# Kernel optimization log

Measured on AMD Instinct MI355X. Metric: run time of the kernel, lower is better.

Reference implementation:

```python
import jax, jax.numpy as jnp
import numpy as np

B, T, L, H, NH, F, V, K = 8, 128, 12, 768, 12, 3072, 30522, 5
DH = H // NH
START, STOP = 3, 4  # tag_to_idx['<START>'], tag_to_idx['<STOP>']


def _ln(x, s, b):
    m = jnp.mean(x, -1, keepdims=True)
    v = jnp.var(x, -1, keepdims=True)
    return (x - m) * jax.lax.rsqrt(v + 1e-12) * s + b


def setup_inputs() -> dict:
    key = jax.random.key(0)
    ks = jax.random.split(key, 16)
    sc = 0.02
    rn = lambda k, shp: jax.random.normal(k, shp, jnp.float32) * sc
    inp = {
        'sentence': jax.random.randint(ks[0], (B, T), 0, V),
        'sentence_mask': jnp.ones((B, T), jnp.int32),
        'word_emb': rn(ks[1], (V, H)),
        'pos_emb': rn(ks[2], (T, H)),
        'type_emb': rn(ks[3], (2, H)),
        'emb_ln_s': jnp.ones((H,), jnp.float32),
        'emb_ln_b': jnp.zeros((H,), jnp.float32),
        'Wqkv': rn(ks[4], (L, H, 3 * H)), 'bqkv': jnp.zeros((L, 3 * H), jnp.float32),
        'Wo': rn(ks[5], (L, H, H)), 'bo': jnp.zeros((L, H), jnp.float32),
        'ln1_s': jnp.ones((L, H), jnp.float32), 'ln1_b': jnp.zeros((L, H), jnp.float32),
        'W1': rn(ks[6], (L, H, F)), 'b1': jnp.zeros((L, F), jnp.float32),
        'W2': rn(ks[7], (L, F, H)), 'b2': jnp.zeros((L, H), jnp.float32),
        'ln2_s': jnp.ones((L, H), jnp.float32), 'ln2_b': jnp.zeros((L, H), jnp.float32),
        'Wt': rn(ks[8], (H, K)), 'bt': jnp.zeros((K,), jnp.float32),
    }
    trans = jax.random.normal(ks[9], (K, K), jnp.float32)
    # transitions[START, :] = -10000 ; transitions[:, STOP] = -10000
    trans = trans.at[START, :].set(-10000.0).at[:, STOP].set(-10000.0)
    inp['transitions'] = trans
    return inp


def _bert_feats(sentence, sentence_mask, word_emb, pos_emb, type_emb,
                emb_ln_s, emb_ln_b, Wqkv, bqkv, Wo, bo, ln1_s, ln1_b,
                W1, b1, W2, b2, ln2_s, ln2_b, Wt, bt):
    # embeddings (token_type_ids=None -> all zeros)
    x = word_emb[sentence] + pos_emb[None, :, :] + type_emb[0][None, None, :]
    x = _ln(x, emb_ln_s, emb_ln_b)
    # additive attention bias from padding mask
    bias = (1.0 - sentence_mask.astype(jnp.float32))[:, None, None, :] * -10000.0
    inv_sqrt_dh = 1.0 / np.sqrt(DH)

    def layer(h, p):
        wqkv, bqk, wo, bo_, s1, sb1, w1, wb1, w2, wb2, s2, sb2 = p
        qkv = h @ wqkv + bqk
        q, k, v = jnp.split(qkv, 3, axis=-1)
        q = q.reshape(B, T, NH, DH)
        k = k.reshape(B, T, NH, DH)
        v = v.reshape(B, T, NH, DH)
        att = jnp.einsum('bqhd,bkhd->bhqk', q, k) * inv_sqrt_dh + bias
        att = jax.nn.softmax(att, axis=-1)
        ctx = jnp.einsum('bhqk,bkhd->bqhd', att, v).reshape(B, T, H)
        h = _ln(h + ctx @ wo + bo_, s1, sb1)
        ff = jax.nn.gelu(h @ w1 + wb1) @ w2 + wb2
        h = _ln(h + ff, s2, sb2)
        return h, None

    x, _ = jax.lax.scan(layer, x, (Wqkv, bqkv, Wo, bo, ln1_s, ln1_b,
                                   W1, b1, W2, b2, ln2_s, ln2_b))
    # dropout(p=0.2) is identity at inference
    return x @ Wt + bt  # [B, T, K]


def _viterbi(feats, transitions):
    # feats: [B, T, K]; transitions[to, from]
    init = jnp.full((B, K), -10000.0, feats.dtype).at[:, START].set(0.0)

    def fwd_step(ld, feat_t):
        m = transitions[None, :, :] + ld[:, None, :]  # [B, K(to), K(from)]
        best = jnp.max(m, axis=-1)
        psi_t = jnp.argmax(m, axis=-1)
        return best + feat_t, psi_t

    feats_t = jnp.swapaxes(feats, 0, 1)  # [T, B, K]
    ld, psis = jax.lax.scan(fwd_step, init, feats_t[1:])  # psis: [T-1, B, K]
    score = jnp.max(ld, axis=-1)          # [B]
    last = jnp.argmax(ld, axis=-1)        # [B]

    def bwd_step(p, psi_t):
        prev = jnp.take_along_axis(psi_t, p[:, None], axis=-1)[:, 0]
        return prev, prev

    _, rest = jax.lax.scan(bwd_step, last, psis, reverse=True)  # [T-1, B]
    path = jnp.concatenate([rest, last[None, :]], axis=0).T     # [B, T]
    return score, path


def reference(sentence, sentence_mask, word_emb, pos_emb, type_emb,
              emb_ln_s, emb_ln_b, Wqkv, bqkv, Wo, bo, ln1_s, ln1_b,
              W1, b1, W2, b2, ln2_s, ln2_b, Wt, bt, transitions):
    feats = _bert_feats(sentence, sentence_mask, word_emb, pos_emb, type_emb,
                        emb_ln_s, emb_ln_b, Wqkv, bqkv, Wo, bo, ln1_s, ln1_b,
                        W1, b1, W2, b2, ln2_s, ln2_b, Wt, bt)
    score, path = _viterbi(feats, transitions)
    return score, path
```

## Files before the change

### kernel.cpp

```cpp
#include <hip/hip_runtime.h>
#include <cstdint>
#include <cstddef>

#define BB 8
#define TT 128
#define LL 12
#define HH 768
#define NHH 12
#define DHH 64
#define FFI 3072
#define KT 5
#define START_TAG 3
#define MTOK (BB*TT)

#define LQS 1769472u
#define LOS 589824u
#define L1S 2359296u
#define L2S 2359296u

typedef _Float16 f16x8 __attribute__((ext_vector_type(8)));
typedef _Float16 f16x4 __attribute__((ext_vector_type(4)));
typedef float f32x4 __attribute__((ext_vector_type(4)));

__device__ __forceinline__ void gl_lds16(const _Float16* g, _Float16* l) {
    __builtin_amdgcn_global_load_lds(
        (const __attribute__((address_space(1))) unsigned int*)g,
        (__attribute__((address_space(3))) unsigned int*)l, 16, 0, 0);
}

__device__ __forceinline__ float gelu_f(float x) {
    float c = 0.7978845608028654f * (x + 0.044715f * x * x * x);
    return 0.5f * x * (1.f + tanhf(c));
}

__device__ __forceinline__ void write_h_planes(const float* rowbuf, int tok,
                                               _Float16* dh, _Float16* dl, int c) {
    int kb = c >> 2;
    int rowm = tok & 127, mb = tok >> 7;
    int koct = c & 3;
    int p = rowm * 4 + (koct ^ (rowm & 3));
    size_t tb = ((size_t)(mb * 24 + kb)) * 4096;
    f16x8 vh, vl;
#pragma unroll
    for (int j = 0; j < 8; ++j) {
        float x = rowbuf[c * 8 + j];
        _Float16 hi = (_Float16)x;
        vh[j] = hi;
        vl[j] = (_Float16)((x - (float)hi) * 4096.f);
    }
    *(f16x8*)(dh + tb + (size_t)p * 8) = vh;
    *(f16x8*)(dl + tb + (size_t)p * 8) = vl;
}

__global__ __launch_bounds__(256) void embed_ln_kernel(
    const int* __restrict__ sentence,
    const float* __restrict__ word_emb,
    const float* __restrict__ pos_emb,
    const float* __restrict__ type_emb,
    const float* __restrict__ ln_s,
    const float* __restrict__ ln_b,
    float* __restrict__ h,
    _Float16* __restrict__ dh, _Float16* __restrict__ dl)
{
    int tok = blockIdx.x;
    int t = tok % TT;
    int id = sentence[tok];
    const float* we = word_emb + (size_t)id * HH;
    const float* pe = pos_emb + (size_t)t * HH;

    __shared__ float rowbuf[HH];
    __shared__ float rs_[4], rss_[4];
    float x[3];
    float s = 0.f, ss = 0.f;
#pragma unroll
    for (int i = 0; i < 3; ++i) {
        int d = threadIdx.x + i * 256;
        float v = we[d] + pe[d] + type_emb[d];
        x[i] = v; s += v; ss += v * v;
    }
    for (int o = 32; o; o >>= 1) { s += __shfl_down(s, o); ss += __shfl_down(ss, o); }
    int wid = threadIdx.x >> 6;
    if ((threadIdx.x & 63) == 0) { rs_[wid] = s; rss_[wid] = ss; }
    __syncthreads();
    s = rs_[0] + rs_[1] + rs_[2] + rs_[3];
    ss = rss_[0] + rss_[1] + rss_[2] + rss_[3];
    float mean = s * (1.f / HH);
    float var = ss * (1.f / HH) - mean * mean;
    float rstd = rsqrtf(var + 1e-12f);
#pragma unroll
    for (int i = 0; i < 3; ++i) {
        int d = threadIdx.x + i * 256;
        float y = (x[i] - mean) * rstd * ln_s[d] + ln_b[d];
        h[(size_t)tok * HH + d] = y;
        rowbuf[d] = y;
    }
    __syncthreads();
    if (threadIdx.x < 96) write_h_planes(rowbuf, tok, dh, dl, threadIdx.x);
}

template<int FEATS>
__global__ __launch_bounds__(256) void add_ln_red_kernel(
    float* __restrict__ h, const float* __restrict__ parts,
    const float* __restrict__ bias,
    const float* __restrict__ ln_s, const float* __restrict__ ln_b,
    _Float16* __restrict__ dh, _Float16* __restrict__ dl,
    const float* __restrict__ Wt, const float* __restrict__ bt,
    float* __restrict__ feats)
{
    int tok = blockIdx.x;
    __shared__ float rowbuf[HH];
    __shared__ float rs_[4], rss_[4];
    float x[3];
    float s = 0.f, ss = 0.f;
#pragma unroll
    for (int i = 0; i < 3; ++i) {
        int d = threadIdx.x + i * 256;
        size_t idx = (size_t)tok * HH + d;
        float delta = parts[idx] + parts[idx + (size_t)MTOK * HH]
                    + parts[idx + 2 * (size_t)MTOK * HH] + parts[idx + 3 * (size_t)MTOK * HH]
                    + bias[d];
        float v = h[idx] + delta;
        x[i] = v; s += v; ss += v * v;
    }
    for (int o = 32; o; o >>= 1) { s += __shfl_down(s, o); ss += __shfl_down(ss, o); }
    int wid = threadIdx.x >> 6;
    if ((threadIdx.x & 63) == 0) { rs_[wid] = s; rss_[wid] = ss; }
    __syncthreads();
    s = rs_[0] + rs_[1] + rs_[2] + rs_[3];
    ss = rss_[0] + rss_[1] + rss_[2] + rss_[3];
    float mean = s * (1.f / HH);
    float var = ss * (1.f / HH) - mean * mean;
    float rstd = rsqrtf(var + 1e-12f);
    float yv[3];
#pragma unroll
    for (int i = 0; i < 3; ++i) {
        int d = threadIdx.x + i * 256;
        float y = (x[i] - mean) * rstd * ln_s[d] + ln_b[d];
        yv[i] = y;
        if constexpr (!FEATS) {
            h[(size_t)tok * HH + d] = y;
            rowbuf[d] = y;
        }
    }
    if constexpr (!FEATS) {
        __syncthreads();
        if (threadIdx.x < 96) write_h_planes(rowbuf, tok, dh, dl, threadIdx.x);
    } else {
        float pt[5] = {0.f, 0.f, 0.f, 0.f, 0.f};
#pragma unroll
        for (int i = 0; i < 3; ++i) {
            int d = threadIdx.x + i * 256;
#pragma unroll
            for (int t = 0; t < 5; ++t) pt[t] += yv[i] * Wt[d * 5 + t];
        }
#pragma unroll
        for (int t = 0; t < 5; ++t)
            for (int o = 32; o; o >>= 1) pt[t] += __shfl_down(pt[t], o);
        __shared__ float fred[4][5];
        if ((threadIdx.x & 63) == 0)
#pragma unroll
            for (int t = 0; t < 5; ++t) fred[wid][t] = pt[t];
        __syncthreads();
        if (threadIdx.x < 5) {
            float fs = fred[0][threadIdx.x] + fred[1][threadIdx.x]
                     + fred[2][threadIdx.x] + fred[3][threadIdx.x] + bt[threadIdx.x];
            feats[tok * 5 + threadIdx.x] = fs;
        }
    }
}

template<int ALL>
__global__ __launch_bounds__(256) void wconv_kernel(
    const float* __restrict__ Wqkv, const float* __restrict__ Wo,
    const float* __restrict__ W1, const float* __restrict__ W2,
    _Float16* __restrict__ qh, _Float16* __restrict__ ql,
    _Float16* __restrict__ oh, _Float16* __restrict__ ol,
    _Float16* __restrict__ f1h, _Float16* __restrict__ f1l,
    _Float16* __restrict__ f2h, _Float16* __restrict__ f2l)
{
    int bb = blockIdx.x;
    int l = ALL ? bb / 3456 : 0;
    int b = ALL ? bb % 3456 : bb;
    const float* src; _Float16 *dh, *dl; int N, kTi, idx;
    if (b < 864)       { idx = b;        src = Wqkv + (size_t)l * 768 * 2304; dh = qh  + (size_t)l * LQS; dl = ql  + (size_t)l * LQS; N = 2304; kTi = 24; }
    else if (b < 1152) { idx = b - 864;  src = Wo   + (size_t)l * 768 * 768;  dh = oh  + (size_t)l * LOS; dl = ol  + (size_t)l * LOS; N = 768;  kTi = 24; }
    else if (b < 2304) { idx = b - 1152; src = W1   + (size_t)l * 768 * 3072; dh = f1h + (size_t)l * L1S; dl = f1l + (size_t)l * L1S; N = 3072; kTi = 24; }
    else               { idx = b - 2304; src = W2   + (size_t)l * 3072 * 768; dh = f2h + (size_t)l * L2S; dl = f2l + (size_t)l * L2S; N = 768;  kTi = 96; }
    int nb = idx / kTi, kb = idx % kTi;

    __shared__ float tile[32][65];
    const float* s0 = src + (size_t)(kb * 32) * N + nb * 64;
#pragma unroll
    for (int i = 0; i < 8; ++i) {
        int q = threadIdx.x + i * 256;
        int kk = q >> 6, n = q & 63;
        tile[kk][n] = s0[(size_t)kk * N + n];
    }
    __syncthreads();
    int p = threadIdx.x;
    int n = p >> 2, koct = (p & 3) ^ (n & 3);
    f16x8 vh, vl;
#pragma unroll
    for (int j = 0; j < 8; ++j) {
        float x = tile[koct * 8 + j][n];
        _Float16 hi = (_Float16)x;
        vh[j] = hi;
        vl[j] = (_Float16)((x - (float)hi) * 4096.f);
    }
    size_t tb = (size_t)idx * 2048;
    *(f16x8*)(dh + tb + (size_t)p * 8) = vh;
    *(f16x8*)(dl + tb + (size_t)p * 8) = vl;
}

template<int MODE>
__global__ __launch_bounds__(256) void mfma_gemm(
    const _Float16* __restrict__ Ah, const _Float16* __restrict__ Al,
    const _Float16* __restrict__ Bh, const _Float16* __restrict__ Bl,
    const float* __restrict__ bias, float* __restrict__ outF,
    _Float16* __restrict__ o1h, _Float16* __restrict__ o1l,
    _Float16* __restrict__ o2h, _Float16* __restrict__ o2l,
    int N, int kTi, int kpz)
{
    constexpr bool TRANS = (MODE >= 2);
    __shared__ _Float16 lds[2][12288];
    int tid = threadIdx.x, lane = tid & 63, w = tid >> 6;
    int wm = w >> 1, wn = w & 1;
    int mb = blockIdx.y, nb = blockIdx.x;
    int ktBeg = TRANS ? 0 : blockIdx.z * kpz;
    int ktEnd = TRANS ? kTi : ktBeg + kpz;

    const _Float16 *aTh, *aTl, *bTh, *bTl;
    if constexpr (!TRANS) {
        aTh = Ah + (size_t)mb * kTi * 4096;
        aTl = Al + (size_t)mb * kTi * 4096;
        bTh = Bh + (size_t)nb * kTi * 2048;
        bTl = Bl + (size_t)nb * kTi * 2048;
    } else {
        aTh = Ah + (size_t)(2 * mb) * kTi * 2048;
        aTl = Al + (size_t)(2 * mb) * kTi * 2048;
        bTh = Bh + (size_t)(nb >> 1) * kTi * 4096 + (nb & 1) * 2048;
        bTl = Bl + (size_t)(nb >> 1) * kTi * 4096 + (nb & 1) * 2048;
    }

    f32x4 acch[4][2], accc[4][2];
#pragma unroll
    for (int i = 0; i < 4; ++i)
#pragma unroll
        for (int j = 0; j < 2; ++j) { acch[i][j] = (f32x4)0.f; accc[i][j] = (f32x4)0.f; }

    auto stage = [&](int buf, int kt) {
#pragma unroll
        for (int j = 0; j < 6; ++j) {
            int i = w * 6 + j;
            const _Float16* src;
            if constexpr (!TRANS) {
                if (i < 8)       src = aTh + (size_t)kt * 4096 + i * 512;
                else if (i < 16) src = aTl + (size_t)kt * 4096 + (i - 8) * 512;
                else if (i < 20) src = bTh + (size_t)kt * 2048 + (i - 16) * 512;
                else             src = bTl + (size_t)kt * 2048 + (i - 20) * 512;
            } else {
                if (i < 8)       src = aTh + (size_t)(i >> 2) * kTi * 2048 + (size_t)kt * 2048 + (i & 3) * 512;
                else if (i < 16) src = aTl + (size_t)((i - 8) >> 2) * kTi * 2048 + (size_t)kt * 2048 + ((i - 8) & 3) * 512;
                else if (i < 20) src = bTh + (size_t)kt * 4096 + (i - 16) * 512;
                else             src = bTl + (size_t)kt * 4096 + (i - 20) * 512;
            }
            gl_lds16(src + lane * 8, &lds[buf][i * 512]);
        }
    };

    stage(0, ktBeg);
    stage(1, ktBeg + 1);
    int lm = lane & 15, lk = lane >> 4;
    for (int kt = ktBeg; kt < ktEnd; ++kt) {
        int cur = (kt - ktBeg) & 1;
        if (kt + 1 < ktEnd) { asm volatile("s_waitcnt vmcnt(6)" ::: "memory"); }
        else                { asm volatile("s_waitcnt vmcnt(0)" ::: "memory"); }
        __builtin_amdgcn_s_barrier();
        __builtin_amdgcn_sched_barrier(0);
        const char* lb = (const char*)&lds[cur][0];
        f16x8 ahf[4], alf[4], bhf[2], blf[2];
#pragma unroll
        for (int mi = 0; mi < 4; ++mi) {
            int row = wm * 64 + mi * 16 + lm;
            int off = (row * 64 + lk * 16) ^ ((row & 3) << 4);
            ahf[mi] = *(const f16x8*)(lb + off);
            alf[mi] = *(const f16x8*)(lb + 8192 + off);
        }
#pragma unroll
        for (int ni = 0; ni < 2; ++ni) {
            int nr = wn * 32 + ni * 16 + lm;
            int off = (nr * 64 + lk * 16) ^ ((nr & 3) << 4);
            bhf[ni] = *(const f16x8*)(lb + 16384 + off);
            blf[ni] = *(const f16x8*)(lb + 20480 + off);
        }
#pragma unroll
        for (int mi = 0; mi < 4; ++mi)
#pragma unroll
            for (int ni = 0; ni < 2; ++ni) {
                acch[mi][ni] = __builtin_amdgcn_mfma_f32_16x16x32_f16(ahf[mi], bhf[ni], acch[mi][ni], 0, 0, 0);
                accc[mi][ni] = __builtin_amdgcn_mfma_f32_16x16x32_f16(ahf[mi], blf[ni], accc[mi][ni], 0, 0, 0);
                accc[mi][ni] = __builtin_amdgcn_mfma_f32_16x16x32_f16(alf[mi], bhf[ni], accc[mi][ni], 0, 0, 0);
            }
        __builtin_amdgcn_sched_barrier(0);
        __builtin_amdgcn_s_barrier();
        if (kt + 2 < ktEnd) stage(cur, kt + 2);
    }

    const float inv = 1.0f / 4096.0f;
    if constexpr (MODE == 0) {
        float* Cz = outF + (size_t)blockIdx.z * 1024 * N;
#pragma unroll
        for (int mi = 0; mi < 4; ++mi)
#pragma unroll
            for (int ni = 0; ni < 2; ++ni) {
                int col = nb * 64 + wn * 32 + ni * 16 + lm;
                int r0 = mb * 128 + wm * 64 + mi * 16 + lk * 4;
#pragma unroll
                for (int j = 0; j < 4; ++j)
                    Cz[(size_t)(r0 + j) * N + col] = acch[mi][ni][j] + accc[mi][ni][j] * inv;
            }
    } else if constexpr (MODE == 2) {
        int region = mb / 6;
#pragma unroll
        for (int mi = 0; mi < 4; ++mi)
#pragma unroll
            for (int ni = 0; ni < 2; ++ni) {
                int n = mb * 128 + wm * 64 + mi * 16 + lk * 4;
                int tok = nb * 64 + wn * 32 + ni * 16 + lm;
                float4 bv = *(const float4*)(bias + n);
                float v[4];
#pragma unroll
                for (int j = 0; j < 4; ++j)
                    v[j] = acch[mi][ni][j] + accc[mi][ni][j] * inv + (&bv.x)[j];
                int b = tok >> 7, q = tok & 127;
                if (region < 2) {
                    int hh2 = (n >> 6) % 12, d = n & 63;
                    size_t img = (size_t)(b * 12 + hh2);
                    _Float16* dsth = (region == 0) ? o1h : o2h;
                    _Float16* dstl = (region == 0) ? o1l : o2l;
                    int byteo = q * 128 + ((d * 2) ^ ((q & 7) << 4));
                    f16x4 hi, lo;
#pragma unroll
                    for (int j = 0; j < 4; ++j) {
                        _Float16 hv = (_Float16)v[j];
                        hi[j] = hv; lo[j] = (_Float16)((v[j] - (float)hv) * 4096.f);
                    }
                    *(f16x4*)((char*)dsth + img * 16384 + byteo) = hi;
                    *(f16x4*)((char*)dstl + img * 16384 + byteo) = lo;
                } else {
                    int hh2 = (n - 1536) >> 6, d = n & 63;
                    float* vdst = outF + (size_t)(b * 12 + hh2) * 8192;
#pragma unroll
                    for (int j = 0; j < 4; ++j)
                        vdst[(size_t)(d + j) * 128 + q] = v[j];
                }
            }
    } else {
#pragma unroll
        for (int mi = 0; mi < 4; ++mi)
#pragma unroll
            for (int ni = 0; ni < 2; ++ni) {
                int n = mb * 128 + wm * 64 + mi * 16 + lk * 4;
                int tok = nb * 64 + wn * 32 + ni * 16 + lm;
                float4 bv = *(const float4*)(bias + n);
                int mbt = tok >> 7, rowm = tok & 127;
                int kb = n >> 5, koct = (n >> 3) & 3, half = (n >> 2) & 1;
                size_t eo = ((size_t)(mbt * 96 + kb)) * 4096
                          + (size_t)(rowm * 4 + (koct ^ (rowm & 3))) * 8 + half * 4;
                f16x4 hi, lo;
#pragma unroll
                for (int j = 0; j < 4; ++j) {
                    float x = gelu_f(acch[mi][ni][j] + accc[mi][ni][j] * inv + (&bv.x)[j]);
                    _Float16 hv = (_Float16)x;
                    hi[j] = hv; lo[j] = (_Float16)((x - (float)hv) * 4096.f);
                }
                *(f16x4*)(o1h + eo) = hi;
                *(f16x4*)(o1l + eo) = lo;
            }
    }
}

__global__ __launch_bounds__(256, 1) void attn_mfma(
    const _Float16* __restrict__ Qp_h, const _Float16* __restrict__ Qp_l,
    const _Float16* __restrict__ Kp_h, const _Float16* __restrict__ Kp_l,
    const float* __restrict__ vT, const int* __restrict__ mask,
    _Float16* __restrict__ cA_h, _Float16* __restrict__ cA_l)
{
    __shared__ __align__(16) char sm[82432];
    char* Kh  = sm;             char* Klo = sm + 16384;
    char* Qh  = sm + 32768;     char* Qlo = sm + 40960;
    char* Ph  = sm;             char* Plo = sm + 16384;
    char* Vth = sm + 49152;     char* Vtl = sm + 65536;
    float* biasf = (float*)(sm + 81920);

    int bx = blockIdx.x;
    int bh = bx >> 1, qh2 = bx & 1;
    int b = bh / 12, h = bh % 12;
    int q0 = qh2 * 64;
    int tid = threadIdx.x, lane = tid & 63, wv = tid >> 6;
    int lm = lane & 15, g = lane >> 4;
    int qr = wv * 16 + lm;
    const float inv = 1.0f / 4096.0f;

    {
        const _Float16* Ksh = Kp_h + (size_t)bh * 8192;
        const _Float16* Ksl = Kp_l + (size_t)bh * 8192;
        const _Float16* Qsh = Qp_h + (size_t)bh * 8192 + (size_t)q0 * 64;
        const _Float16* Qsl = Qp_l + (size_t)bh * 8192 + (size_t)q0 * 64;
#pragma unroll
        for (int i = 0; i < 4; ++i) {
            gl_lds16(Ksh + (size_t)(i * 256 + tid) * 8, (_Float16*)(Kh  + (i * 256 + tid) * 16));
            gl_lds16(Ksl + (size_t)(i * 256 + tid) * 8, (_Float16*)(Klo + (i * 256 + tid) * 16));
        }
#pragma unroll
        for (int i = 0; i < 2; ++i) {
            gl_lds16(Qsh + (size_t)(i * 256 + tid) * 8, (_Float16*)(Qh  + (i * 256 + tid) * 16));
            gl_lds16(Qsl + (size_t)(i * 256 + tid) * 8, (_Float16*)(Qlo + (i * 256 + tid) * 16));
        }
    }
    if (tid < 128) biasf[tid] = (1.f - (float)mask[b * 128 + tid]) * -10000.f;
    __syncthreads();

    f32x4 ah[8], ac[8];
#pragma unroll
    for (int i = 0; i < 8; ++i) { ah[i] = (f32x4)0.f; ac[i] = (f32x4)0.f; }
    __builtin_amdgcn_s_setprio(1);
#pragma unroll
    for (int ks = 0; ks < 2; ++ks) {
        int qoff = qr * 128 + ((ks * 64 + g * 16) ^ ((qr & 7) << 4));
        f16x8 q_h = *(const f16x8*)(Qh + qoff);
        f16x8 q_l = *(const f16x8*)(Qlo + qoff);
#pragma unroll
        for (int mf = 0; mf < 8; ++mf) {
            int kt = mf * 16 + lm;
            int koff = kt * 128 + ((ks * 64 + g * 16) ^ ((kt & 7) << 4));
            f16x8 k_h = *(const f16x8*)(Kh + koff);
            f16x8 k_l = *(const f16x8*)(Klo + koff);
            ah[mf] = __builtin_amdgcn_mfma_f32_16x16x32_f16(k_h, q_h, ah[mf], 0, 0, 0);
            ac[mf] = __builtin_amdgcn_mfma_f32_16x16x32_f16(k_h, q_l, ac[mf], 0, 0, 0);
            ac[mf] = __builtin_amdgcn_mfma_f32_16x16x32_f16(k_l, q_h, ac[mf], 0, 0, 0);
        }
    }
    __builtin_amdgcn_s_setprio(0);

    float kb_[8][4];
#pragma unroll
    for (int mf = 0; mf < 8; ++mf)
#pragma unroll
        for (int jj = 0; jj < 4; ++jj) kb_[mf][jj] = biasf[mf * 16 + g * 4 + jj];

    float pv_[8][4];
    float mx = -1e30f;
#pragma unroll
    for (int mf = 0; mf < 8; ++mf)
#pragma unroll
        for (int jj = 0; jj < 4; ++jj) {
            float s = (ah[mf][jj] + ac[mf][jj] * inv) * 0.125f + kb_[mf][jj];
            pv_[mf][jj] = s;
            mx = fmaxf(mx, s);
        }
    mx = fmaxf(mx, __shfl_xor(mx, 16));
    mx = fmaxf(mx, __shfl_xor(mx, 32));
    float sum = 0.f;
#pragma unroll
    for (int mf = 0; mf < 8; ++mf)
#pragma unroll
        for (int jj = 0; jj < 4; ++jj) {
            float e = expf(pv_[mf][jj] - mx);
            pv_[mf][jj] = e;
            sum += e;
        }
    sum += __shfl_xor(sum, 16);
    sum += __shfl_xor(sum, 32);
    float rs = 1.f / sum;
    __syncthreads();

#pragma unroll
    for (int mf = 0; mf < 8; ++mf) {
        f16x4 hi, lo;
#pragma unroll
        for (int jj = 0; jj < 4; ++jj) {
            float p = pv_[mf][jj] * rs;
            _Float16 hv = (_Float16)p;
            hi[jj] = hv; lo[jj] = (_Float16)((p - (float)hv) * 4096.f);
        }
        int byteo = qr * 256 + ((mf * 32 + g * 8) ^ ((qr & 7) << 4));
        *(f16x4*)(Ph + byteo) = hi;
        *(f16x4*)(Plo + byteo) = lo;
    }
    {
        int d = tid >> 2, tb = (tid & 3) * 32;
        const float* vsrc = vT + (size_t)bh * 8192 + (size_t)d * 128 + tb;
#pragma unroll
        for (int i = 0; i < 8; ++i) {
            float4 v = *(const float4*)(vsrc + i * 4);
            f16x4 hi, lo;
#pragma unroll
            for (int jj = 0; jj < 4; ++jj) {
                float x = (&v.x)[jj];
                _Float16 hv = (_Float16)x;
                hi[jj] = hv; lo[jj] = (_Float16)((x - (float)hv) * 4096.f);
            }
            int byteo = d * 256 + (((tb + i * 4) * 2) ^ ((d & 7) << 4));
            *(f16x4*)(Vth + byteo) = hi;
            *(f16x4*)(Vtl + byteo) = lo;
        }
    }
    __syncthreads();

    f32x4 ch[4], cc[4];
#pragma unroll
    for (int i = 0; i < 4; ++i) { ch[i] = (f32x4)0.f; cc[i] = (f32x4)0.f; }
    __builtin_amdgcn_s_setprio(1);
#pragma unroll
    for (int ks = 0; ks < 4; ++ks) {
        int poff = qr * 256 + ((ks * 64 + g * 16) ^ ((qr & 7) << 4));
        f16x8 p_h = *(const f16x8*)(Ph + poff);
        f16x8 p_l = *(const f16x8*)(Plo + poff);
#pragma unroll
        for (int mf = 0; mf < 4; ++mf) {
            int d = mf * 16 + lm;
            int voff = d * 256 + ((ks * 64 + g * 16) ^ ((d & 7) << 4));
            f16x8 vh = *(const f16x8*)(Vth + voff);
            f16x8 vl = *(const f16x8*)(Vtl + voff);
            ch[mf] = __builtin_amdgcn_mfma_f32_16x16x32_f16(vh, p_h, ch[mf], 0, 0, 0);
            cc[mf] = __builtin_amdgcn_mfma_f32_16x16x32_f16(vh, p_l, cc[mf], 0, 0, 0);
            cc[mf] = __builtin_amdgcn_mfma_f32_16x16x32_f16(vl, p_h, cc[mf], 0, 0, 0);
        }
    }
    __builtin_amdgcn_s_setprio(0);

    int q = q0 + qr;
#pragma unroll
    for (int mf = 0; mf < 4; ++mf) {
        int d0 = mf * 16 + g * 4;
        f16x4 hi, lo;
#pragma unroll
        for (int jj = 0; jj < 4; ++jj) {
            float x = ch[mf][jj] + cc[mf][jj] * inv;
            _Float16 hv = (_Float16)x;
            hi[jj] = hv; lo[jj] = (_Float16)((x - (float)hv) * 4096.f);
        }
        int kb = h * 2 + (d0 >> 5), koct = (d0 >> 3) & 3, half = (d0 >> 2) & 1;
        size_t eo = ((size_t)(b * 24 + kb)) * 4096
                  + (size_t)(q * 4 + (koct ^ (q & 3))) * 8 + half * 4;
        *(f16x4*)(cA_h + eo) = hi;
        *(f16x4*)(cA_l + eo) = lo;
    }
}

__global__ __launch_bounds__(64) void viterbi_kernel(
    const float* __restrict__ feats, const float* __restrict__ trans,
    float* __restrict__ out)
{
    __shared__ float tr[KT][KT];
    __shared__ unsigned char psi[TT - 1][BB][KT];
    int tid = threadIdx.x;
    if (tid < KT * KT) tr[tid / KT][tid % KT] = trans[tid];
    __syncthreads();
    if (tid < BB) {
        int b = tid;
        float ld[KT];
#pragma unroll
        for (int k = 0; k < KT; ++k) ld[k] = (k == START_TAG) ? 0.f : -10000.f;
        for (int t = 1; t < TT; ++t) {
            float nld[KT];
#pragma unroll
            for (int to = 0; to < KT; ++to) {
                float best = tr[to][0] + ld[0];
                int arg = 0;
#pragma unroll
                for (int fr = 1; fr < KT; ++fr) {
                    float v = tr[to][fr] + ld[fr];
                    if (v > best) { best = v; arg = fr; }
                }
                psi[t - 1][b][to] = (unsigned char)arg;
                nld[to] = best + feats[(size_t)(b * TT + t) * KT + to];
            }
#pragma unroll
            for (int k = 0; k < KT; ++k) ld[k] = nld[k];
        }
        float sc = ld[0]; int last = 0;
#pragma unroll
        for (int k = 1; k < KT; ++k) if (ld[k] > sc) { sc = ld[k]; last = k; }
        out[b] = sc;
        int p = last;
        out[BB + b * TT + (TT - 1)] = (float)last;
        for (int t = TT - 2; t >= 0; --t) {
            p = psi[t][b][p];
            out[BB + b * TT + t] = (float)p;
        }
    }
}

extern "C" void kernel_launch(void* const* d_in, const int* in_sizes, int n_in,
                              void* d_out, int out_size, void* d_ws, size_t ws_size,
                              hipStream_t stream) {
    const int*   sentence = (const int*)d_in[0];
    const int*   mask     = (const int*)d_in[1];
    const float* word_emb = (const float*)d_in[2];
    const float* pos_emb  = (const float*)d_in[3];
    const float* type_emb = (const float*)d_in[4];
    const float* emb_ln_s = (const float*)d_in[5];
    const float* emb_ln_b = (const float*)d_in[6];
    const float* Wqkv     = (const float*)d_in[7];
    const float* bqkv     = (const float*)d_in[8];
    const float* Wo       = (const float*)d_in[9];
    const float* bo       = (const float*)d_in[10];
    const float* ln1_s    = (const float*)d_in[11];
    const float* ln1_b    = (const float*)d_in[12];
    const float* W1       = (const float*)d_in[13];
    const float* b1       = (const float*)d_in[14];
    const float* W2       = (const float*)d_in[15];
    const float* b2       = (const float*)d_in[16];
    const float* ln2_s    = (const float*)d_in[17];
    const float* ln2_b    = (const float*)d_in[18];
    const float* Wt       = (const float*)d_in[19];
    const float* bt       = (const float*)d_in[20];
    const float* trans    = (const float*)d_in[21];

    char* base = (char*)d_ws;
    size_t off = 0;
    auto alloc = [&](size_t bytes) { void* p = base + off; off += (bytes + 255) & ~(size_t)255; return p; };

    const size_t planeElems = (size_t)(LQS + LOS + L1S + L2S);
    bool allL = ws_size >= (planeElems * 12 * 2 * 2 + (size_t)120 * 1024 * 1024);
    int NLL = allL ? 12 : 1;

    _Float16* wq_h = (_Float16*)alloc((size_t)LQS * NLL * 2);
    _Float16* wq_l = (_Float16*)alloc((size_t)LQS * NLL * 2);
    _Float16* wo_h = (_Float16*)alloc((size_t)LOS * NLL * 2);
    _Float16* wo_l = (_Float16*)alloc((size_t)LOS * NLL * 2);
    _Float16* w1_h = (_Float16*)alloc((size_t)L1S * NLL * 2);
    _Float16* w1_l = (_Float16*)alloc((size_t)L1S * NLL * 2);
    _Float16* w2_h = (_Float16*)alloc((size_t)L2S * NLL * 2);
    _Float16* w2_l = (_Float16*)alloc((size_t)L2S * NLL * 2);
    float* h       = (float*)alloc((size_t)MTOK * HH * 4);
    _Float16* hA_h = (_Float16*)alloc((size_t)MTOK * HH * 2);
    _Float16* hA_l = (_Float16*)alloc((size_t)MTOK * HH * 2);
    _Float16* Qp_h = (_Float16*)alloc((size_t)96 * 8192 * 2);
    _Float16* Qp_l = (_Float16*)alloc((size_t)96 * 8192 * 2);
    _Float16* Kp_h = (_Float16*)alloc((size_t)96 * 8192 * 2);
    _Float16* Kp_l = (_Float16*)alloc((size_t)96 * 8192 * 2);
    float* vT      = (float*)alloc((size_t)96 * 8192 * 4);
    _Float16* cA_h = (_Float16*)alloc((size_t)MTOK * HH * 2);
    _Float16* cA_l = (_Float16*)alloc((size_t)MTOK * HH * 2);
    _Float16* gA_h = (_Float16*)alloc((size_t)MTOK * FFI * 2);
    _Float16* gA_l = (_Float16*)alloc((size_t)MTOK * FFI * 2);
    float* parts   = (float*)alloc((size_t)4 * MTOK * HH * 4);
    float* featsb  = (float*)alloc((size_t)MTOK * KT * 4);

    embed_ln_kernel<<<MTOK, 256, 0, stream>>>(sentence, word_emb, pos_emb, type_emb,
                                              emb_ln_s, emb_ln_b, h, hA_h, hA_l);
    if (allL) {
        wconv_kernel<1><<<41472, 256, 0, stream>>>(
            Wqkv, Wo, W1, W2,
            wq_h, wq_l, wo_h, wo_l, w1_h, w1_l, w2_h, w2_l);
    }
    for (int l = 0; l < LL; ++l) {
        size_t qO = allL ? (size_t)l * LQS : 0;
        size_t oO = allL ? (size_t)l * LOS : 0;
        size_t f1O = allL ? (size_t)l * L1S : 0;
        size_t f2O = allL ? (size_t)l * L2S : 0;
        if (!allL) {
            wconv_kernel<0><<<3456, 256, 0, stream>>>(
                Wqkv + (size_t)l * 768 * 2304, Wo + (size_t)l * 768 * 768,
                W1 + (size_t)l * 768 * 3072, W2 + (size_t)l * 3072 * 768,
                wq_h, wq_l, wo_h, wo_l, w1_h, w1_l, w2_h, w2_l);
        }
        mfma_gemm<2><<<dim3(16, 18), 256, 0, stream>>>(
            wq_h + qO, wq_l + qO, hA_h, hA_l, bqkv + (size_t)l * 2304, vT,
            Qp_h, Qp_l, Kp_h, Kp_l, 0, 24, 24);
        attn_mfma<<<192, 256, 0, stream>>>(Qp_h, Qp_l, Kp_h, Kp_l, vT, mask, cA_h, cA_l);
        mfma_gemm<0><<<dim3(12, 8, 4), 256, 0, stream>>>(
            cA_h, cA_l, wo_h + oO, wo_l + oO, nullptr, parts,
            nullptr, nullptr, nullptr, nullptr, 768, 24, 6);
        add_ln_red_kernel<0><<<MTOK, 256, 0, stream>>>(
            h, parts, bo + (size_t)l * HH, ln1_s + (size_t)l * HH, ln1_b + (size_t)l * HH,
            hA_h, hA_l, nullptr, nullptr, nullptr);
        mfma_gemm<3><<<dim3(16, 24), 256, 0, stream>>>(
            w1_h + f1O, w1_l + f1O, hA_h, hA_l, b1 + (size_t)l * FFI, nullptr,
            gA_h, gA_l, nullptr, nullptr, 0, 24, 24);
        mfma_gemm<0><<<dim3(12, 8, 4), 256, 0, stream>>>(
            gA_h, gA_l, w2_h + f2O, w2_l + f2O, nullptr, parts,
            nullptr, nullptr, nullptr, nullptr, 768, 96, 24);
        if (l < LL - 1) {
            add_ln_red_kernel<0><<<MTOK, 256, 0, stream>>>(
                h, parts, b2 + (size_t)l * HH, ln2_s + (size_t)l * HH, ln2_b + (size_t)l * HH,
                hA_h, hA_l, nullptr, nullptr, nullptr);
        } else {
            add_ln_red_kernel<1><<<MTOK, 256, 0, stream>>>(
                h, parts, b2 + (size_t)l * HH, ln2_s + (size_t)l * HH, ln2_b + (size_t)l * HH,
                hA_h, hA_l, Wt, bt, featsb);
        }
    }
    viterbi_kernel<<<1, 64, 0, stream>>>(featsb, trans, (float*)d_out);
}
```

Measured before the change: 1.543 ms.

## Fuse all encoder layers into one persistent cooperative kernel with grid syncs

```diff
diff --git a/kernel.cpp b/kernel.cpp
--- a/kernel.cpp
+++ b/kernel.cpp
@@ -1,6 +1,9 @@
 #include <hip/hip_runtime.h>
+#include <hip/hip_cooperative_groups.h>
 #include <cstdint>
 #include <cstddef>
+
+namespace cg = cooperative_groups;
 
 #define BB 8
 #define TT 128
@@ -99,17 +102,18 @@
 }
 
 template<int FEATS>
-__global__ __launch_bounds__(256) void add_ln_red_kernel(
-    float* __restrict__ h, const float* __restrict__ parts,
-    const float* __restrict__ bias,
-    const float* __restrict__ ln_s, const float* __restrict__ ln_b,
-    _Float16* __restrict__ dh, _Float16* __restrict__ dl,
-    const float* __restrict__ Wt, const float* __restrict__ bt,
-    float* __restrict__ feats)
-{
-    int tok = blockIdx.x;
-    __shared__ float rowbuf[HH];
-    __shared__ float rs_[4], rss_[4];
+__device__ __forceinline__ void ln_body(
+    char* smemc, float* h, const float* parts, const float* bias,
+    const float* ln_s, const float* ln_b,
+    _Float16* dh, _Float16* dl,
+    const float* Wt, const float* bt, float* feats, int tok)
+{
+    float* rowbuf = (float*)smemc;
+    float* rs_ = (float*)(smemc + 3072);
+    float* rss_ = (float*)(smemc + 3088);
+    float (*fred)[5] = (float (*)[5])(smemc + 3104);
+    __syncthreads();
+
     float x[3];
     float s = 0.f, ss = 0.f;
 #pragma unroll
@@ -156,7 +160,6 @@
 #pragma unroll
         for (int t = 0; t < 5; ++t)
             for (int o = 32; o; o >>= 1) pt[t] += __shfl_down(pt[t], o);
-        __shared__ float fred[4][5];
         if ((threadIdx.x & 63) == 0)
 #pragma unroll
             for (int t = 0; t < 5; ++t) fred[wid][t] = pt[t];
@@ -167,6 +170,17 @@
             feats[tok * 5 + threadIdx.x] = fs;
         }
     }
+}
+
+template<int FEATS>
+__global__ __launch_bounds__(256) void add_ln_red_kernel(
+    float* h, const float* parts, const float* bias,
+    const float* ln_s, const float* ln_b,
+    _Float16* dh, _Float16* dl,
+    const float* Wt, const float* bt, float* feats)
+{
+    __shared__ __align__(16) char smem[3200];
+    ln_body<FEATS>(smem, h, parts, bias, ln_s, ln_b, dh, dl, Wt, bt, feats, blockIdx.x);
 }
 
 template<int ALL>
@@ -213,20 +227,20 @@
 }
 
 template<int MODE>
-__global__ __launch_bounds__(256) void mfma_gemm(
+__device__ __forceinline__ void gemm_tile(
+    char* smemc,
     const _Float16* __restrict__ Ah, const _Float16* __restrict__ Al,
     const _Float16* __restrict__ Bh, const _Float16* __restrict__ Bl,
     const float* __restrict__ bias, float* __restrict__ outF,
     _Float16* __restrict__ o1h, _Float16* __restrict__ o1l,
     _Float16* __restrict__ o2h, _Float16* __restrict__ o2l,
-    int N, int kTi, int kpz)
+    int N, int kTi, int kpz, int mb, int nb, int zz)
 {
     constexpr bool TRANS = (MODE >= 2);
-    __shared__ _Float16 lds[2][12288];
+    _Float16* lds = (_Float16*)smemc;
     int tid = threadIdx.x, lane = tid & 63, w = tid >> 6;
     int wm = w >> 1, wn = w & 1;
-    int mb = blockIdx.y, nb = blockIdx.x;
-    int ktBeg = TRANS ? 0 : blockIdx.z * kpz;
+    int ktBeg = TRANS ? 0 : zz * kpz;
     int ktEnd = TRANS ? kTi : ktBeg + kpz;
 
     const _Float16 *aTh, *aTl, *bTh, *bTl;
@@ -264,7 +278,7 @@
                 else if (i < 20) src = bTh + (size_t)kt * 4096 + (i - 16) * 512;
                 else             src = bTl + (size_t)kt * 4096 + (i - 20) * 512;
             }
-            gl_lds16(src + lane * 8, &lds[buf][i * 512]);
+            gl_lds16(src + lane * 8, &lds[buf * 12288 + i * 512]);
         }
     };
 
@@ -277,7 +291,7 @@
         else                { asm volatile("s_waitcnt vmcnt(0)" ::: "memory"); }
         __builtin_amdgcn_s_barrier();
         __builtin_amdgcn_sched_barrier(0);
-        const char* lb = (const char*)&lds[cur][0];
+        const char* lb = (const char*)&lds[cur * 12288];
         f16x8 ahf[4], alf[4], bhf[2], blf[2];
 #pragma unroll
         for (int mi = 0; mi < 4; ++mi) {
@@ -308,7 +322,7 @@
 
     const float inv = 1.0f / 4096.0f;
     if constexpr (MODE == 0) {
-        float* Cz = outF + (size_t)blockIdx.z * 1024 * N;
+        float* Cz = outF + (size_t)zz * 1024 * N;
 #pragma unroll
         for (int mi = 0; mi < 4; ++mi)
 #pragma unroll
@@ -380,20 +394,32 @@
     }
 }
 
-__global__ __launch_bounds__(256, 1) void attn_mfma(
+template<int MODE>
+__global__ __launch_bounds__(256) void mfma_gemm(
+    const _Float16* Ah, const _Float16* Al,
+    const _Float16* Bh, const _Float16* Bl,
+    const float* bias, float* outF,
+    _Float16* o1h, _Float16* o1l, _Float16* o2h, _Float16* o2l,
+    int N, int kTi, int kpz)
+{
+    __shared__ __align__(16) char smem[49152];
+    gemm_tile<MODE>(smem, Ah, Al, Bh, Bl, bias, outF, o1h, o1l, o2h, o2l,
+                    N, kTi, kpz, blockIdx.y, blockIdx.x, blockIdx.z);
+}
+
+__device__ __forceinline__ void attn_body(
+    char* sm,
     const _Float16* __restrict__ Qp_h, const _Float16* __restrict__ Qp_l,
     const _Float16* __restrict__ Kp_h, const _Float16* __restrict__ Kp_l,
     const float* __restrict__ vT, const int* __restrict__ mask,
-    _Float16* __restrict__ cA_h, _Float16* __restrict__ cA_l)
-{
-    __shared__ __align__(16) char sm[82432];
+    _Float16* __restrict__ cA_h, _Float16* __restrict__ cA_l, int bx)
+{
     char* Kh  = sm;             char* Klo = sm + 16384;
     char* Qh  = sm + 32768;     char* Qlo = sm + 40960;
     char* Ph  = sm;             char* Plo = sm + 16384;
     char* Vth = sm + 49152;     char* Vtl = sm + 65536;
     float* biasf = (float*)(sm + 81920);
 
-    int bx = blockIdx.x;
     int bh = bx >> 1, qh2 = bx & 1;
     int b = bh / 12, h = bh % 12;
     int q0 = qh2 * 64;
@@ -402,6 +428,7 @@
     int qr = wv * 16 + lm;
     const float inv = 1.0f / 4096.0f;
 
+    __syncthreads();
     {
         const _Float16* Ksh = Kp_h + (size_t)bh * 8192;
         const _Float16* Ksl = Kp_l + (size_t)bh * 8192;
@@ -546,6 +573,93 @@
                   + (size_t)(q * 4 + (koct ^ (q & 3))) * 8 + half * 4;
         *(f16x4*)(cA_h + eo) = hi;
         *(f16x4*)(cA_l + eo) = lo;
+    }
+}
+
+__global__ __launch_bounds__(256, 1) void attn_mfma(
+    const _Float16* Qp_h, const _Float16* Qp_l,
+    const _Float16* Kp_h, const _Float16* Kp_l,
+    const float* vT, const int* mask,
+    _Float16* cA_h, _Float16* cA_l)
+{
+    __shared__ __align__(16) char sm[82432];
+    attn_body(sm, Qp_h, Qp_l, Kp_h, Kp_l, vT, mask, cA_h, cA_l, blockIdx.x);
+}
+
+struct MegaArgs {
+    const int* mask;
+    const float *bqkv, *bo, *b1, *b2, *ln1_s, *ln1_b, *ln2_s, *ln2_b, *Wt, *bt;
+    const _Float16 *wq_h, *wq_l, *wo_h, *wo_l, *w1_h, *w1_l, *w2_h, *w2_l;
+    float* h;
+    _Float16 *hA_h, *hA_l;
+    _Float16 *Qp_h, *Qp_l, *Kp_h, *Kp_l;
+    float* vT;
+    _Float16 *cA_h, *cA_l, *gA_h, *gA_l;
+    float* parts;
+    float* feats;
+};
+
+__global__ __launch_bounds__(256, 1) void mega_kernel(MegaArgs a)
+{
+    __shared__ __align__(16) char smem[82432];
+    cg::grid_group grid = cg::this_grid();
+
+    for (int l = 0; l < LL; ++l) {
+        const _Float16* wqh = a.wq_h + (size_t)l * LQS;
+        const _Float16* wql = a.wq_l + (size_t)l * LQS;
+        const _Float16* woh = a.wo_h + (size_t)l * LOS;
+        const _Float16* wol = a.wo_l + (size_t)l * LOS;
+        const _Float16* w1h = a.w1_h + (size_t)l * L1S;
+        const _Float16* w1l = a.w1_l + (size_t)l * L1S;
+        const _Float16* w2h = a.w2_h + (size_t)l * L2S;
+        const _Float16* w2l = a.w2_l + (size_t)l * L2S;
+
+        for (int idx = blockIdx.x; idx < 288; idx += gridDim.x)
+            gemm_tile<2>(smem, wqh, wql, a.hA_h, a.hA_l, a.bqkv + (size_t)l * 2304, a.vT,
+                         a.Qp_h, a.Qp_l, a.Kp_h, a.Kp_l, 2304, 24, 24, idx / 16, idx % 16, 0);
+        grid.sync();
+
+        for (int bx = blockIdx.x; bx < 192; bx += gridDim.x)
+            attn_body(smem, a.Qp_h, a.Qp_l, a.Kp_h, a.Kp_l, a.vT, a.mask, a.cA_h, a.cA_l, bx);
+        grid.sync();
+
+        for (int idx = blockIdx.x; idx < 384; idx += gridDim.x) {
+            int zz = idx / 96, r = idx % 96;
+            gemm_tile<0>(smem, a.cA_h, a.cA_l, woh, wol, nullptr, a.parts,
+                         nullptr, nullptr, nullptr, nullptr, 768, 24, 6, r / 12, r % 12, zz);
+        }
+        grid.sync();
+
+        for (int tok = blockIdx.x; tok < 1024; tok += gridDim.x)
+            ln_body<0>(smem, a.h, a.parts, a.bo + (size_t)l * HH,
+                       a.ln1_s + (size_t)l * HH, a.ln1_b + (size_t)l * HH,
+                       a.hA_h, a.hA_l, nullptr, nullptr, nullptr, tok);
+        grid.sync();
+
+        for (int idx = blockIdx.x; idx < 384; idx += gridDim.x)
+            gemm_tile<3>(smem, w1h, w1l, a.hA_h, a.hA_l, a.b1 + (size_t)l * FFI, nullptr,
+                         a.gA_h, a.gA_l, nullptr, nullptr, 3072, 24, 24, idx / 16, idx % 16, 0);
+        grid.sync();
+
+        for (int idx = blockIdx.x; idx < 384; idx += gridDim.x) {
+            int zz = idx / 96, r = idx % 96;
+            gemm_tile<0>(smem, a.gA_h, a.gA_l, w2h, w2l, nullptr, a.parts,
+                         nullptr, nullptr, nullptr, nullptr, 768, 96, 24, r / 12, r % 12, zz);
+        }
+        grid.sync();
+
+        if (l < LL - 1) {
+            for (int tok = blockIdx.x; tok < 1024; tok += gridDim.x)
+                ln_body<0>(smem, a.h, a.parts, a.b2 + (size_t)l * HH,
+                           a.ln2_s + (size_t)l * HH, a.ln2_b + (size_t)l * HH,
+                           a.hA_h, a.hA_l, nullptr, nullptr, nullptr, tok);
+        } else {
+            for (int tok = blockIdx.x; tok < 1024; tok += gridDim.x)
+                ln_body<1>(smem, a.h, a.parts, a.b2 + (size_t)l * HH,
+                           a.ln2_s + (size_t)l * HH, a.ln2_b + (size_t)l * HH,
+                           a.hA_h, a.hA_l, a.Wt, a.bt, a.feats, tok);
+        }
+        grid.sync();
     }
 }
 
@@ -623,8 +737,7 @@
     size_t off = 0;
     auto alloc = [&](size_t bytes) { void* p = base + off; off += (bytes + 255) & ~(size_t)255; return p; };
 
-    const size_t planeElems = (size_t)(LQS + LOS + L1S + L2S);
-    bool allL = ws_size >= (planeElems * 12 * 2 * 2 + (size_t)120 * 1024 * 1024);
+    bool allL = ws_size >= (384ULL << 20);
     int NLL = allL ? 12 : 1;
 
     _Float16* wq_h = (_Float16*)alloc((size_t)LQS * NLL * 2);
@@ -652,46 +765,65 @@
 
     embed_ln_kernel<<<MTOK, 256, 0, stream>>>(sentence, word_emb, pos_emb, type_emb,
                                               emb_ln_s, emb_ln_b, h, hA_h, hA_l);
+
+    bool megaDone = false;
     if (allL) {
         wconv_kernel<1><<<41472, 256, 0, stream>>>(
-            Wqkv, Wo, W1, W2,
-            wq_h, wq_l, wo_h, wo_l, w1_h, w1_l, w2_h, w2_l);
-    }
-    for (int l = 0; l < LL; ++l) {
-        size_t qO = allL ? (size_t)l * LQS : 0;
-        size_t oO = allL ? (size_t)l * LOS : 0;
-        size_t f1O = allL ? (size_t)l * L1S : 0;
-        size_t f2O = allL ? (size_t)l * L2S : 0;
-        if (!allL) {
-            wconv_kernel<0><<<3456, 256, 0, stream>>>(
-                Wqkv + (size_t)l * 768 * 2304, Wo + (size_t)l * 768 * 768,
-                W1 + (size_t)l * 768 * 3072, W2 + (size_t)l * 3072 * 768,
-                wq_h, wq_l, wo_h, wo_l, w1_h, w1_l, w2_h, w2_l);
-        }
-        mfma_gemm<2><<<dim3(16, 18), 256, 0, stream>>>(
-            wq_h + qO, wq_l + qO, hA_h, hA_l, bqkv + (size_t)l * 2304, vT,
-            Qp_h, Qp_l, Kp_h, Kp_l, 0, 24, 24);
-        attn_mfma<<<192, 256, 0, stream>>>(Qp_h, Qp_l, Kp_h, Kp_l, vT, mask, cA_h, cA_l);
-        mfma_gemm<0><<<dim3(12, 8, 4), 256, 0, stream>>>(
-            cA_h, cA_l, wo_h + oO, wo_l + oO, nullptr, parts,
-            nullptr, nullptr, nullptr, nullptr, 768, 24, 6);
-        add_ln_red_kernel<0><<<MTOK, 256, 0, stream>>>(
-            h, parts, bo + (size_t)l * HH, ln1_s + (size_t)l * HH, ln1_b + (size_t)l * HH,
-            hA_h, hA_l, nullptr, nullptr, nullptr);
-        mfma_gemm<3><<<dim3(16, 24), 256, 0, stream>>>(
-            w1_h + f1O, w1_l + f1O, hA_h, hA_l, b1 + (size_t)l * FFI, nullptr,
-            gA_h, gA_l, nullptr, nullptr, 0, 24, 24);
-        mfma_gemm<0><<<dim3(12, 8, 4), 256, 0, stream>>>(
-            gA_h, gA_l, w2_h + f2O, w2_l + f2O, nullptr, parts,
-            nullptr, nullptr, nullptr, nullptr, 768, 96, 24);
-        if (l < LL - 1) {
+            Wqkv, Wo, W1, W2, wq_h, wq_l, wo_h, wo_l, w1_h, w1_l, w2_h, w2_l);
+        MegaArgs ma;
+        ma.mask = mask;
+        ma.bqkv = bqkv; ma.bo = bo; ma.b1 = b1; ma.b2 = b2;
+        ma.ln1_s = ln1_s; ma.ln1_b = ln1_b; ma.ln2_s = ln2_s; ma.ln2_b = ln2_b;
+        ma.Wt = Wt; ma.bt = bt;
+        ma.wq_h = wq_h; ma.wq_l = wq_l; ma.wo_h = wo_h; ma.wo_l = wo_l;
+        ma.w1_h = w1_h; ma.w1_l = w1_l; ma.w2_h = w2_h; ma.w2_l = w2_l;
+        ma.h = h; ma.hA_h = hA_h; ma.hA_l = hA_l;
+        ma.Qp_h = Qp_h; ma.Qp_l = Qp_l; ma.Kp_h = Kp_h; ma.Kp_l = Kp_l;
+        ma.vT = vT; ma.cA_h = cA_h; ma.cA_l = cA_l; ma.gA_h = gA_h; ma.gA_l = gA_l;
+        ma.parts = parts; ma.feats = featsb;
+        void* kp[1] = { &ma };
+        hipError_t ce = hipLaunchCooperativeKernel((const void*)mega_kernel,
+                                                   dim3(256), dim3(256), kp, 0, stream);
+        if (ce == hipSuccess) megaDone = true;
+    }
+
+    if (!megaDone) {
+        for (int l = 0; l < LL; ++l) {
+            size_t qO = allL ? (size_t)l * LQS : 0;
+            size_t oO = allL ? (size_t)l * LOS : 0;
+            size_t f1O = allL ? (size_t)l * L1S : 0;
+            size_t f2O = allL ? (size_t)l * L2S : 0;
+            if (!allL) {
+                wconv_kernel<0><<<3456, 256, 0, stream>>>(
+                    Wqkv + (size_t)l * 768 * 2304, Wo + (size_t)l * 768 * 768,
+                    W1 + (size_t)l * 768 * 3072, W2 + (size_t)l * 3072 * 768,
+                    wq_h, wq_l, wo_h, wo_l, w1_h, w1_l, w2_h, w2_l);
+            }
+            mfma_gemm<2><<<dim3(16, 18), 256, 0, stream>>>(
+                wq_h + qO, wq_l + qO, hA_h, hA_l, bqkv + (size_t)l * 2304, vT,
+                Qp_h, Qp_l, Kp_h, Kp_l, 2304, 24, 24);
+            attn_mfma<<<192, 256, 0, stream>>>(Qp_h, Qp_l, Kp_h, Kp_l, vT, mask, cA_h, cA_l);
+            mfma_gemm<0><<<dim3(12, 8, 4), 256, 0, stream>>>(
+                cA_h, cA_l, wo_h + oO, wo_l + oO, nullptr, parts,
+                nullptr, nullptr, nullptr, nullptr, 768, 24, 6);
             add_ln_red_kernel<0><<<MTOK, 256, 0, stream>>>(
-                h, parts, b2 + (size_t)l * HH, ln2_s + (size_t)l * HH, ln2_b + (size_t)l * HH,
+                h, parts, bo + (size_t)l * HH, ln1_s + (size_t)l * HH, ln1_b + (size_t)l * HH,
                 hA_h, hA_l, nullptr, nullptr, nullptr);
-        } else {
-            add_ln_red_kernel<1><<<MTOK, 256, 0, stream>>>(
-                h, parts, b2 + (size_t)l * HH, ln2_s + (size_t)l * HH, ln2_b + (size_t)l * HH,
-                hA_h, hA_l, Wt, bt, featsb);
+            mfma_gemm<3><<<dim3(16, 24), 256, 0, stream>>>(
+                w1_h + f1O, w1_l + f1O, hA_h, hA_l, b1 + (size_t)l * FFI, nullptr,
+                gA_h, gA_l, nullptr, nullptr, 3072, 24, 24);
+            mfma_gemm<0><<<dim3(12, 8, 4), 256, 0, stream>>>(
+                gA_h, gA_l, w2_h + f2O, w2_l + f2O, nullptr, parts,
+                nullptr, nullptr, nullptr, nullptr, 768, 96, 24);
+            if (l < LL - 1) {
+                add_ln_red_kernel<0><<<MTOK, 256, 0, stream>>>(
+                    h, parts, b2 + (size_t)l * HH, ln2_s + (size_t)l * HH, ln2_b + (size_t)l * HH,
+                    hA_h, hA_l, nullptr, nullptr, nullptr);
+            } else {
+                add_ln_red_kernel<1><<<MTOK, 256, 0, stream>>>(
+                    h, parts, b2 + (size_t)l * HH, ln2_s + (size_t)l * HH, ln2_b + (size_t)l * HH,
+                    hA_h, hA_l, Wt, bt, featsb);
+            }
         }
     }
     viterbi_kernel<<<1, 64, 0, stream>>>(featsb, trans, (float*)d_out);
```

After: 4.883 ms. 3.16x slower.
